# Kernel optimization log

Hardware: AMD Instinct MI355X
Metric: run time of the kernel (lower is better)

## Reference

```python
import jax, jax.numpy as jnp
import numpy as np

N_NODES = 50000
N_EDGES = 800000
IN_DIM = 32
EMBED_DIM = 64
OUT_DIM = 1
N_LAYERS = 8


def setup_inputs() -> dict:
    key = jax.random.key(0)
    ks = jax.random.split(key, 10)
    x = jax.random.normal(ks[0], (N_NODES, IN_DIM), dtype=jnp.float32)
    src = jax.random.randint(ks[1], (N_EDGES,), 0, N_NODES, dtype=jnp.int32)
    dst = jax.random.randint(ks[2], (N_EDGES,), 0, N_NODES, dtype=jnp.int32)
    # learned params
    s_in = 1.0 / np.sqrt(IN_DIM)
    s_d = 1.0 / np.sqrt(EMBED_DIM)
    W_embed = jax.random.uniform(ks[3], (IN_DIM, EMBED_DIM), jnp.float32, -s_in, s_in)
    b_embed = jnp.zeros((EMBED_DIM,), jnp.float32)
    Ws = jax.random.uniform(ks[4], (N_LAYERS, EMBED_DIM, EMBED_DIM), jnp.float32, -s_d, s_d)
    bs = jnp.zeros((N_LAYERS, EMBED_DIM), jnp.float32)
    W_dec = jax.random.uniform(ks[5], (EMBED_DIM, OUT_DIM), jnp.float32, -s_d, s_d)
    b_dec = jnp.zeros((OUT_DIM,), jnp.float32)
    return {"x": x, "src": src, "dst": dst, "W_embed": W_embed, "b_embed": b_embed,
            "Ws": Ws, "bs": bs, "W_dec": W_dec, "b_dec": b_dec}


def reference(x, src, dst, W_embed, b_embed, Ws, bs, W_dec, b_dec):
    N = x.shape[0]
    ones = jnp.ones(src.shape[0], x.dtype)
    # DGL GraphConv norm='both': degrees clamped to min 1
    deg_out = jnp.maximum(jax.ops.segment_sum(ones, src, num_segments=N), 1.0)
    deg_in = jnp.maximum(jax.ops.segment_sum(ones, dst, num_segments=N), 1.0)
    inv_out = deg_out ** -0.5  # [N]
    inv_in = deg_in ** -0.5    # [N]

    h = x @ W_embed + b_embed  # [N, D]

    def layer(h, wb):
        W, b = wb
        m = (h * inv_out[:, None])[src]                      # gather [E, D]
        agg = jax.ops.segment_sum(m, dst, num_segments=N)    # scatter-add [N, D]
        h = (agg * inv_in[:, None]) @ W + b
        return h, None

    h, _ = jax.lax.scan(layer, h, (Ws, bs))
    return h @ W_dec + b_dec  # [N, OUT_DIM]
```

## Files before the change

### kernel.cpp

```cpp
#include <hip/hip_runtime.h>


#define PAD 48

__global__ __launch_bounds__(256) void prep_kernel(
        const float* __restrict__ W_embed, const float* __restrict__ b_embed,
        const float* __restrict__ Ws, const float* __restrict__ bs,
        const float* __restrict__ W_dec, float* __restrict__ coef,
        int* __restrict__ cnt, int N2) {
    int g = blockIdx.x * 256 + threadIdx.x;
    for (int i = g; i < N2; i += gridDim.x * 256) cnt[i] = 0;
    if (blockIdx.x == 0) {
        __shared__ float shv[64];
        __shared__ float shg[9];
        int i = threadIdx.x;
        if (i < 64) shv[i] = W_dec[i];
        __syncthreads();
        for (int l = 7; l >= 0; --l) {
            float a = 0.f;
            if (i < 64) {
                float p = bs[l * 64 + i] * shv[i];
                for (int d = 32; d; d >>= 1) p += __shfl_xor(p, d);
                if (i == 0) shg[l + 1] = p;
                const float* Wrow = Ws + l * 4096 + i * 64;
                for (int j = 0; j < 64; ++j) a += Wrow[j] * shv[j];
            }
            __syncthreads();
            if (i < 64) shv[i] = a;
            __syncthreads();
        }
        if (i < 64) {
            float p = b_embed[i] * shv[i];
            for (int d = 32; d; d >>= 1) p += __shfl_xor(p, d);
            if (i == 0) shg[0] = p;
        }
        __syncthreads();
        if (i < 32) {
            float a = 0.f;
            const float* Wr = W_embed + i * 64;
            for (int j = 0; j < 64; ++j) a += Wr[j] * shv[j];
            coef[16 + i] = a;
        }
        if (i < 9) coef[i] = shg[i];
    }
}

__global__ __launch_bounds__(256) void fill_kernel(
        const int* __restrict__ src, const int* __restrict__ dst,
        int* __restrict__ cnt_out, int* __restrict__ cursor,
        unsigned short* __restrict__ csr, int E) {
    int i = blockIdx.x * 256 + threadIdx.x;
    if (i >= E) return;
    int s = src[i], d = dst[i];
    atomicAdd(&cnt_out[s], 1);
    int p = atomicAdd(&cursor[d], 1);
    if (p < PAD) csr[(size_t)d * PAD + p] = (unsigned short)s;
}

__global__ __launch_bounds__(256) void z0_kernel(
        const float* __restrict__ x, const float* __restrict__ coef,
        const int* __restrict__ cnt_out, const int* __restrict__ cursor,
        float* __restrict__ inv_out, float* __restrict__ inv_in,
        float* __restrict__ ts0, int N) {
    __shared__ float w[33];
    if (threadIdx.x < 32) w[threadIdx.x] = coef[16 + threadIdx.x];
    if (threadIdx.x == 32) w[32] = coef[0];
    __syncthreads();
    int n = blockIdx.x * 256 + threadIdx.x;
    if (n >= N) return;
    const float4* xr = (const float4*)(x + (size_t)n * 32);
    float acc = 0.f;
#pragma unroll
    for (int q = 0; q < 8; ++q) {
        float4 vv = xr[q];
        acc += vv.x * w[q * 4] + vv.y * w[q * 4 + 1] + vv.z * w[q * 4 + 2] + vv.w * w[q * 4 + 3];
    }
    int co = cnt_out[n]; if (co < 1) co = 1;
    int ci = cursor[n];  if (ci < 1) ci = 1;
    float io = rsqrtf((float)co);
    inv_out[n] = io;
    inv_in[n] = rsqrtf((float)ci);
    ts0[n] = io * (acc + w[32]);
}

__device__ __forceinline__ float quad_gather(const unsigned short* __restrict__ row,
                                             const float* __restrict__ ta,
                                             int c, int sub) {
    float acc = 0.f;
#pragma unroll
    for (int t = 0; t < PAD / 16; ++t) {
        int eb = sub * 4 + 16 * t;
        if (eb < c) {
            uint2 v = *(const uint2*)(row + eb);
            unsigned i0 = v.x & 0xFFFF, i1 = v.x >> 16;
            unsigned i2 = v.y & 0xFFFF, i3 = v.y >> 16;
            acc += ta[i0];
            if (eb + 1 < c) acc += ta[i1];
            if (eb + 2 < c) acc += ta[i2];
            if (eb + 3 < c) acc += ta[i3];
        }
    }
    return acc;
}

__global__ __launch_bounds__(256) void prop_kernel(
        const float* __restrict__ ts_in, float* __restrict__ ts_out,
        const float* __restrict__ inv_out, const float* __restrict__ inv_in,
        const int* __restrict__ cursor, const unsigned short* __restrict__ csr,
        const float* __restrict__ coef, int k, int N) {
    int tid = blockIdx.x * 256 + threadIdx.x;
    int n = tid >> 2, sub = tid & 3;
    if (n >= N) return;
    int c = cursor[n]; if (c > PAD) c = PAD;
    float acc = quad_gather(csr + (size_t)n * PAD, ts_in, c, sub);
    acc += __shfl_xor(acc, 1);
    acc += __shfl_xor(acc, 2);
    if (sub == 0) ts_out[n] = inv_out[n] * (inv_in[n] * acc + coef[k]);
}

__global__ __launch_bounds__(256) void final_kernel(
        const float* __restrict__ ts_in, float* __restrict__ out,
        const float* __restrict__ inv_in, const int* __restrict__ cursor,
        const unsigned short* __restrict__ csr, const float* __restrict__ coef,
        const float* __restrict__ b_dec, int N) {
    int tid = blockIdx.x * 256 + threadIdx.x;
    int n = tid >> 2, sub = tid & 3;
    if (n >= N) return;
    int c = cursor[n]; if (c > PAD) c = PAD;
    float acc = quad_gather(csr + (size_t)n * PAD, ts_in, c, sub);
    acc += __shfl_xor(acc, 1);
    acc += __shfl_xor(acc, 2);
    if (sub == 0) out[n] = inv_in[n] * acc + coef[8] + b_dec[0];
}

__global__ __launch_bounds__(256) void fill_kernel_i(
        const int* __restrict__ src, const int* __restrict__ dst,
        int* __restrict__ cnt_out, int* __restrict__ cursor,
        int* __restrict__ csr, int E) {
    int i = blockIdx.x * 256 + threadIdx.x;
    if (i >= E) return;
    int s = src[i], d = dst[i];
    atomicAdd(&cnt_out[s], 1);
    int p = atomicAdd(&cursor[d], 1);
    if (p < PAD) csr[(size_t)d * PAD + p] = s;
}

__global__ __launch_bounds__(256) void prop_kernel_i(
        const float* __restrict__ ts_in, float* __restrict__ ts_out,
        const float* __restrict__ inv_out, const float* __restrict__ inv_in,
        const int* __restrict__ cursor, const int* __restrict__ csr,
        const float* __restrict__ coef, int k, int N) {
    int n = blockIdx.x * 256 + threadIdx.x;
    if (n >= N) return;
    int c = cursor[n]; if (c > PAD) c = PAD;
    const int* row = csr + (size_t)n * PAD;
    float acc = 0.f;
    for (int e = 0; e < c; ++e) acc += ts_in[row[e]];
    ts_out[n] = inv_out[n] * (inv_in[n] * acc + coef[k]);
}

__global__ __launch_bounds__(256) void final_kernel_i(
        const float* __restrict__ ts_in, float* __restrict__ out,
        const float* __restrict__ inv_in, const int* __restrict__ cursor,
        const int* __restrict__ csr, const float* __restrict__ coef,
        const float* __restrict__ b_dec, int N) {
    int n = blockIdx.x * 256 + threadIdx.x;
    if (n >= N) return;
    int c = cursor[n]; if (c > PAD) c = PAD;
    const int* row = csr + (size_t)n * PAD;
    float acc = 0.f;
    for (int e = 0; e < c; ++e) acc += ts_in[row[e]];
    out[n] = inv_in[n] * acc + coef[8] + b_dec[0];
}

extern "C" void kernel_launch(void* const* d_in, const int* in_sizes, int n_in,
                              void* d_out, int out_size, void* d_ws, size_t ws_size,
                              hipStream_t stream) {
    const float* x       = (const float*)d_in[0];
    const int*   src     = (const int*)d_in[1];
    const int*   dst     = (const int*)d_in[2];
    const float* W_embed = (const float*)d_in[3];
    const float* b_embed = (const float*)d_in[4];
    const float* Ws      = (const float*)d_in[5];
    const float* bs      = (const float*)d_in[6];
    const float* W_dec   = (const float*)d_in[7];
    const float* b_dec   = (const float*)d_in[8];
    float* out = (float*)d_out;
    int N = in_sizes[0] / 32;
    int E = in_sizes[1];

    char* w = (char*)d_ws;
    size_t o = 0;
    int* cnt_out = (int*)(w + o); o += (size_t)N * 4;
    int* cursor  = (int*)(w + o); o += (size_t)N * 4;
    o = (o + 255) & ~(size_t)255;
    float* inv_out = (float*)(w + o); o += (size_t)N * 4; o = (o + 255) & ~(size_t)255;
    float* inv_in  = (float*)(w + o); o += (size_t)N * 4; o = (o + 255) & ~(size_t)255;
    float* coef    = (float*)(w + o); o += 256;
    float* tsA     = (float*)(w + o); o += (size_t)N * 4; o = (o + 255) & ~(size_t)255;
    float* tsB     = (float*)(w + o); o += (size_t)N * 4; o = (o + 255) & ~(size_t)255;
    void* csr_mem  = (void*)(w + o);

    int nbl  = (N + 255) / 256;
    int nbl4 = (4 * N + 255) / 256;
    int ebl  = (E + 255) / 256;

    prep_kernel<<<128, 256, 0, stream>>>(W_embed, b_embed, Ws, bs, W_dec, coef, cnt_out, 2 * N);

    if (N <= 65536) {
        unsigned short* csr = (unsigned short*)csr_mem;
        fill_kernel<<<ebl, 256, 0, stream>>>(src, dst, cnt_out, cursor, csr, E);
        z0_kernel<<<nbl, 256, 0, stream>>>(x, coef, cnt_out, cursor, inv_out, inv_in, tsA, N);
        float* ta = tsA; float* tb = tsB;
        for (int k = 1; k <= 7; ++k) {
            prop_kernel<<<nbl4, 256, 0, stream>>>(ta, tb, inv_out, inv_in, cursor, csr, coef, k, N);
            float* tmp = ta; ta = tb; tb = tmp;
        }
        final_kernel<<<nbl4, 256, 0, stream>>>(ta, out, inv_in, cursor, csr, coef, b_dec, N);
    } else {
        int* csr = (int*)csr_mem;
        fill_kernel_i<<<ebl, 256, 0, stream>>>(src, dst, cnt_out, cursor, csr, E);
        z0_kernel<<<nbl, 256, 0, stream>>>(x, coef, cnt_out, cursor, inv_out, inv_in, tsA, N);
        float* ta = tsA; float* tb = tsB;
        for (int k = 1; k <= 7; ++k) {
            prop_kernel_i<<<nbl, 256, 0, stream>>>(ta, tb, inv_out, inv_in, cursor, csr, coef, k, N);
            float* tmp = ta; ta = tb; tb = tmp;
        }
        final_kernel_i<<<nbl, 256, 0, stream>>>(ta, out, inv_in, cursor, csr, coef, b_dec, N);
    }
}
```

Baseline: 143.3 us.

## Replace global out-degree atomics with packed LDS histograms fused into CSR fill

Out-degree counting moves off global atomics. Sixteen extra blocks in the fill kernel each build a shared-memory histogram, with two 16-bit counts packed per word, over one eighth of the edges and half the node range. z0 then sums the eight partial histograms per node. This removes about 800k contended global atomics, at the cost of a few serial histogram blocks running alongside the fill and eight extra reads per node in z0. The large-N path keeps the old scheme through a duplicated z0 kernel.

After: 212.1 us. 1.48x slower.

```diff
diff --git a/kernel.cpp b/kernel.cpp
--- a/kernel.cpp
+++ b/kernel.cpp
@@ -2,14 +2,15 @@
 
 
 #define PAD 48
+#define HB 16
 
 __global__ __launch_bounds__(256) void prep_kernel(
         const float* __restrict__ W_embed, const float* __restrict__ b_embed,
         const float* __restrict__ Ws, const float* __restrict__ bs,
         const float* __restrict__ W_dec, float* __restrict__ coef,
-        int* __restrict__ cnt, int N2) {
+        int* __restrict__ cnt, int NZ) {
     int g = blockIdx.x * 256 + threadIdx.x;
-    for (int i = g; i < N2; i += gridDim.x * 256) cnt[i] = 0;
+    for (int i = g; i < NZ; i += gridDim.x * 256) cnt[i] = 0;
     if (blockIdx.x == 0) {
         __shared__ float shv[64];
         __shared__ float shg[9];
@@ -45,21 +46,40 @@
     }
 }
 
-__global__ __launch_bounds__(256) void fill_kernel(
+__global__ __launch_bounds__(256) void fill_hist_kernel(
         const int* __restrict__ src, const int* __restrict__ dst,
-        int* __restrict__ cnt_out, int* __restrict__ cursor,
-        unsigned short* __restrict__ csr, int E) {
-    int i = blockIdx.x * 256 + threadIdx.x;
-    if (i >= E) return;
-    int s = src[i], d = dst[i];
-    atomicAdd(&cnt_out[s], 1);
-    int p = atomicAdd(&cursor[d], 1);
-    if (p < PAD) csr[(size_t)d * PAD + p] = (unsigned short)s;
+        int* __restrict__ cursor, unsigned short* __restrict__ csr,
+        unsigned* __restrict__ pu, int E) {
+    __shared__ unsigned lds[16384];
+    int b = blockIdx.x;
+    if (b < HB) {
+        int q = b & 7, r = b >> 3;
+        for (int i = threadIdx.x; i < 16384; i += 256) lds[i] = 0;
+        __syncthreads();
+        long long e0 = (long long)E * q / 8;
+        long long e1 = (long long)E * (q + 1) / 8;
+        int base = r << 15;
+        for (long long e = e0 + threadIdx.x; e < e1; e += 256) {
+            int t = src[e] - base;
+            if ((unsigned)t < 32768u)
+                atomicAdd(&lds[t >> 1], 1u << ((t & 1) * 16));
+        }
+        __syncthreads();
+        unsigned* outp = pu + ((size_t)q << 15) + ((size_t)r << 14);
+        for (int i = threadIdx.x; i < 16384; i += 256) outp[i] = lds[i];
+    } else {
+        int i = (b - HB) * 256 + threadIdx.x;
+        if (i < E) {
+            int s = src[i], d = dst[i];
+            int p = atomicAdd(&cursor[d], 1);
+            if (p < PAD) csr[(size_t)d * PAD + p] = (unsigned short)s;
+        }
+    }
 }
 
 __global__ __launch_bounds__(256) void z0_kernel(
         const float* __restrict__ x, const float* __restrict__ coef,
-        const int* __restrict__ cnt_out, const int* __restrict__ cursor,
+        const unsigned* __restrict__ pu, const int* __restrict__ cursor,
         float* __restrict__ inv_out, float* __restrict__ inv_in,
         float* __restrict__ ts0, int N) {
     __shared__ float w[33];
@@ -75,8 +95,12 @@
         float4 vv = xr[q];
         acc += vv.x * w[q * 4] + vv.y * w[q * 4 + 1] + vv.z * w[q * 4 + 2] + vv.w * w[q * 4 + 3];
     }
-    int co = cnt_out[n]; if (co < 1) co = 1;
-    int ci = cursor[n];  if (ci < 1) ci = 1;
+    int j = n >> 1, sh = (n & 1) * 16;
+    int co = 0;
+#pragma unroll
+    for (int q = 0; q < 8; ++q) co += (pu[((size_t)q << 15) + j] >> sh) & 0xFFFF;
+    if (co < 1) co = 1;
+    int ci = cursor[n]; if (ci < 1) ci = 1;
     float io = rsqrtf((float)co);
     inv_out[n] = io;
     inv_in[n] = rsqrtf((float)ci);
@@ -143,6 +167,32 @@
     atomicAdd(&cnt_out[s], 1);
     int p = atomicAdd(&cursor[d], 1);
     if (p < PAD) csr[(size_t)d * PAD + p] = s;
+}
+
+__global__ __launch_bounds__(256) void z0_kernel_i(
+        const float* __restrict__ x, const float* __restrict__ coef,
+        const int* __restrict__ cnt_out, const int* __restrict__ cursor,
+        float* __restrict__ inv_out, float* __restrict__ inv_in,
+        float* __restrict__ ts0, int N) {
+    __shared__ float w[33];
+    if (threadIdx.x < 32) w[threadIdx.x] = coef[16 + threadIdx.x];
+    if (threadIdx.x == 32) w[32] = coef[0];
+    __syncthreads();
+    int n = blockIdx.x * 256 + threadIdx.x;
+    if (n >= N) return;
+    const float4* xr = (const float4*)(x + (size_t)n * 32);
+    float acc = 0.f;
+#pragma unroll
+    for (int q = 0; q < 8; ++q) {
+        float4 vv = xr[q];
+        acc += vv.x * w[q * 4] + vv.y * w[q * 4 + 1] + vv.z * w[q * 4 + 2] + vv.w * w[q * 4 + 3];
+    }
+    int co = cnt_out[n]; if (co < 1) co = 1;
+    int ci = cursor[n];  if (ci < 1) ci = 1;
+    float io = rsqrtf((float)co);
+    inv_out[n] = io;
+    inv_in[n] = rsqrtf((float)ci);
+    ts0[n] = io * (acc + w[32]);
 }
 
 __global__ __launch_bounds__(256) void prop_kernel_i(
@@ -191,9 +241,12 @@
 
     char* w = (char*)d_ws;
     size_t o = 0;
-    int* cnt_out = (int*)(w + o); o += (size_t)N * 4;
-    int* cursor  = (int*)(w + o); o += (size_t)N * 4;
-    o = (o + 255) & ~(size_t)255;
+    int* cursor = (int*)(w + o); o += (size_t)N * 4;
+    size_t region = (size_t)1 << 20;
+    if ((size_t)N * 4 > region) region = (size_t)N * 4;
+    unsigned* pu  = (unsigned*)(w + o);
+    int* cnt_out  = (int*)(w + o);
+    o += region; o = (o + 255) & ~(size_t)255;
     float* inv_out = (float*)(w + o); o += (size_t)N * 4; o = (o + 255) & ~(size_t)255;
     float* inv_in  = (float*)(w + o); o += (size_t)N * 4; o = (o + 255) & ~(size_t)255;
     float* coef    = (float*)(w + o); o += 256;
@@ -205,12 +258,11 @@
     int nbl4 = (4 * N + 255) / 256;
     int ebl  = (E + 255) / 256;
 
-    prep_kernel<<<128, 256, 0, stream>>>(W_embed, b_embed, Ws, bs, W_dec, coef, cnt_out, 2 * N);
-
     if (N <= 65536) {
         unsigned short* csr = (unsigned short*)csr_mem;
-        fill_kernel<<<ebl, 256, 0, stream>>>(src, dst, cnt_out, cursor, csr, E);
-        z0_kernel<<<nbl, 256, 0, stream>>>(x, coef, cnt_out, cursor, inv_out, inv_in, tsA, N);
+        prep_kernel<<<128, 256, 0, stream>>>(W_embed, b_embed, Ws, bs, W_dec, coef, cursor, N);
+        fill_hist_kernel<<<ebl + HB, 256, 0, stream>>>(src, dst, cursor, csr, pu, E);
+        z0_kernel<<<nbl, 256, 0, stream>>>(x, coef, pu, cursor, inv_out, inv_in, tsA, N);
         float* ta = tsA; float* tb = tsB;
         for (int k = 1; k <= 7; ++k) {
             prop_kernel<<<nbl4, 256, 0, stream>>>(ta, tb, inv_out, inv_in, cursor, csr, coef, k, N);
@@ -219,8 +271,9 @@
         final_kernel<<<nbl4, 256, 0, stream>>>(ta, out, inv_in, cursor, csr, coef, b_dec, N);
     } else {
         int* csr = (int*)csr_mem;
+        prep_kernel<<<128, 256, 0, stream>>>(W_embed, b_embed, Ws, bs, W_dec, coef, cursor, 2 * N);
         fill_kernel_i<<<ebl, 256, 0, stream>>>(src, dst, cnt_out, cursor, csr, E);
-        z0_kernel<<<nbl, 256, 0, stream>>>(x, coef, cnt_out, cursor, inv_out, inv_in, tsA, N);
+        z0_kernel_i<<<nbl, 256, 0, stream>>>(x, coef, cnt_out, cursor, inv_out, inv_in, tsA, N);
         float* ta = tsA; float* tb = tsB;
         for (int k = 1; k <= 7; ++k) {
             prop_kernel_i<<<nbl, 256, 0, stream>>>(ta, tb, inv_out, inv_in, cursor, csr, coef, k, N);
```
